# Optimization experiments

Hardware: AMD Instinct MI355X
Metric: run time of the kernel (lower is better)

## Reference

```python
import jax, jax.numpy as jnp
from jax import lax
import numpy as np

B, K_UP, K_DOWN = 32, 64, 192
D, S_UP, S_DOWN, C = 768, 24576, 24576, 256
CHUNK = 64  # connection chunk size (source uses 256; C=256 here, 4 chunks of 64)


def setup_inputs() -> dict:
    key = jax.random.key(0)
    k1, k2, k3, k4, k5, k6, k7 = jax.random.split(key, 7)
    up_decoder = jax.random.normal(k1, (D, S_UP), dtype=jnp.float32) * 0.02
    down_encoder = jax.random.normal(k2, (S_DOWN, D), dtype=jnp.float32) * 0.02
    up_b_dec = jax.random.normal(k3, (D,), dtype=jnp.float32) * 0.02
    up_vals = jax.random.normal(k4, (B, K_UP), dtype=jnp.float32)
    # connection table: indices of connected upstream features, -1 padded.
    conn = jax.random.randint(k5, (S_DOWN, C), 0, S_UP, dtype=jnp.int64)
    pad = jax.random.uniform(jax.random.fold_in(k5, 1), (S_DOWN, C)) < 0.25
    connections = jnp.where(pad, jnp.int64(-1), conn)
    up_indices = jax.random.randint(k6, (B, K_UP), 0, S_UP, dtype=jnp.int64)
    down_indices = jax.random.randint(k7, (B, K_DOWN), 0, S_DOWN, dtype=jnp.int64)
    return {"up_decoder": up_decoder, "down_encoder": down_encoder,
            "up_b_dec": up_b_dec, "up_vals": up_vals,
            "connections": connections, "up_indices": up_indices,
            "down_indices": down_indices}


def reference(up_decoder, down_encoder, up_b_dec, up_vals,
              connections, up_indices, down_indices):
    """JAX port of SCAESuite.get_pruned_contributions."""
    Bb, ku = up_indices.shape
    kd = down_indices.shape[1]
    Cc = connections.shape[1]
    # gather active upstream decoder columns -> [B, k_up, D]
    up_vecs = up_decoder.T[up_indices]
    # gather active downstream encoder rows -> [B, k_down, D]
    down_vecs = down_encoder[down_indices]
    # virtual weights [B, k_down, k_up]
    vw = jnp.einsum('bkd,bud->bku', down_vecs, up_vecs)
    # gather connection rows for each active downstream feature [B, k_down, C]
    conn_down = connections[down_indices]
    # scan over connection chunks, scatter-accumulating masked contributions
    chunks = conn_down.reshape(Bb, kd, Cc // CHUNK, CHUNK).transpose(2, 0, 1, 3)

    def body(acc, conn_chunk):  # conn_chunk [B, k_down, CHUNK]
        valid = conn_chunk != -1
        # match[b, kd, c, ku] = connection c of down feature equals active up feature
        match = (conn_chunk[..., None] == up_indices[:, None, None, :]) & valid[..., None]
        contrib = jnp.sum(
            jnp.where(match, vw[:, :, None, :] * up_vals[:, None, None, :], 0.0),
            axis=(2, 3))
        return acc + contrib, None

    contributions, _ = lax.scan(body, jnp.zeros((Bb, kd), up_vals.dtype), chunks)
    # upstream decoder bias contribution through downstream encoder
    b_dec_contrib = down_encoder @ up_b_dec  # [S_down]
    return contributions + b_dec_contrib[down_indices]
```

## Files before the change

### kernel.cpp

```cpp
#include <hip/hip_runtime.h>
#include <hip/hip_bf16.h>

#define B_SZ     32
#define K_UP     64
#define K_DOWN   192
#define D_DIM    768
#define S_UP     24576
#define C_CONN   256
#define NCOL     (B_SZ * K_UP)
#define MAXM     512
#define BM_WORDS (S_UP / 32)

#define CCH      512
#define RCH      16
#define NCH_C    (S_UP / CCH)
#define NCH_R    (D_DIM / RCH)
#define SLOTS    192

__global__ __launch_bounds__(256) void gather_up_cols_scan(
    const float* __restrict__ up_decoder,
    const int*   __restrict__ up_idx_flat,
    float*       __restrict__ ws_up)
{
    const int tid = threadIdx.x;
    const int c0  = blockIdx.x * CCH;
    const int d0  = blockIdx.y * RCH;

    __shared__ float tile[RCH][CCH + 4];
    __shared__ int   s_j[SLOTS];
    __shared__ int   s_cc[SLOTS];
    __shared__ int   s_cnt;

    if (tid == 0) s_cnt = 0;
    __syncthreads();

    for (int i = tid; i < NCOL; i += 256) {
        const int cc = up_idx_flat[i] - c0;
        if (cc >= 0 && cc < CCH) {
            int slot = atomicAdd(&s_cnt, 1);
            if (slot < SLOTS) { s_j[slot] = i; s_cc[slot] = cc; }
        }
    }

    #pragma unroll
    for (int k = 0; k < 8; ++k) {
        const int lin = k * 256 + tid;
        const int r   = lin >> 7;
        const int c4  = lin & 127;
        float4 v = *(const float4*)&up_decoder[(size_t)(d0 + r) * S_UP + c0 + c4 * 4];
        *(float4*)&tile[r][c4 * 4] = v;
    }
    __syncthreads();

    int cnt = s_cnt; if (cnt > SLOTS) cnt = SLOTS;

    const int q = tid & 3;
    for (int s = tid >> 2; s < cnt; s += 64) {
        const int j  = s_j[s];
        const int cc = s_cc[s];
        float4 v = make_float4(tile[4 * q + 0][cc], tile[4 * q + 1][cc],
                               tile[4 * q + 2][cc], tile[4 * q + 3][cc]);
        *(float4*)&ws_up[(size_t)j * D_DIM + d0 + 4 * q] = v;
    }
}

__global__ __launch_bounds__(256) void scae_pruned_contrib(
    const float* __restrict__ up_decoder,
    const float* __restrict__ ws_up,
    const float* __restrict__ down_encoder,
    const float* __restrict__ up_b_dec,
    const float* __restrict__ up_vals,
    const int*   __restrict__ connections,
    const int*   __restrict__ up_indices,
    const int*   __restrict__ down_indices,
    float*       __restrict__ out,
    const int                 use_ws)
{
    const int tid = threadIdx.x;
    const int blk = blockIdx.x;
    const int b   = blk / K_DOWN;
    const int kd  = blk - b * K_DOWN;

    __shared__ int      s_upidx[K_UP];
    __shared__ float    s_upvals[K_UP];
    __shared__ unsigned s_bm[BM_WORDS];
    __shared__ int      s_ku[MAXM];
    __shared__ float    s_coef[MAXM];
    __shared__ int      s_nm;
    __shared__ float    s_red[4];

    const int dj = down_indices[b * K_DOWN + kd];
    const int v  = connections[(size_t)dj * C_CONN + tid];

    const float* drow = down_encoder + (size_t)dj * D_DIM;
    const float dr0 = drow[tid];
    const float dr1 = drow[tid + 256];
    const float dr2 = drow[tid + 512];

    float c0 = up_b_dec[tid];
    float c1 = up_b_dec[tid + 256];
    float c2 = up_b_dec[tid + 512];

    int   ui = 0;
    float uv = 0.f;
    if (tid < K_UP) {
        ui = up_indices[b * K_UP + tid];
        uv = up_vals[b * K_UP + tid];
    }

    #pragma unroll
    for (int w = 0; w < BM_WORDS / 256; ++w) s_bm[tid + 256 * w] = 0u;
    if (tid == 0) s_nm = 0;
    if (tid < K_UP) { s_upidx[tid] = ui; s_upvals[tid] = uv; }
    __syncthreads();

    if (tid < K_UP) atomicOr(&s_bm[ui >> 5], 1u << (ui & 31));
    __syncthreads();

    if (v >= 0 && ((s_bm[v >> 5] >> (v & 31)) & 1u)) {
        for (int ku = 0; ku < K_UP; ++ku) {
            if (s_upidx[ku] == v) {
                int slot = atomicAdd(&s_nm, 1);
                if (slot < MAXM) {
                    s_ku[slot]   = ku;
                    s_coef[slot] = s_upvals[ku];
                }
            }
        }
    }
    __syncthreads();
    int nm = s_nm;
    if (nm > MAXM) nm = MAXM;

    for (int m = 0; m < nm; ++m) {
        const float coef = s_coef[m];
        const int   ku   = s_ku[m];
        if (use_ws) {
            const float* colp = ws_up + (size_t)(b * K_UP + ku) * D_DIM;
            c0 += coef * colp[tid];
            c1 += coef * colp[tid + 256];
            c2 += coef * colp[tid + 512];
        } else {
            const int col = s_upidx[ku];
            c0 += coef * up_decoder[(size_t)(tid      ) * S_UP + col];
            c1 += coef * up_decoder[(size_t)(tid + 256) * S_UP + col];
            c2 += coef * up_decoder[(size_t)(tid + 512) * S_UP + col];
        }
    }

    float partial = c0 * dr0 + c1 * dr1 + c2 * dr2;

    for (int off = 32; off > 0; off >>= 1)
        partial += __shfl_down(partial, off, 64);
    const int wave = tid >> 6;
    const int lane = tid & 63;
    if (lane == 0) s_red[wave] = partial;
    __syncthreads();
    if (tid == 0) {
        out[blk] = s_red[0] + s_red[1] + s_red[2] + s_red[3];
    }
}

extern "C" void kernel_launch(void* const* d_in, const int* in_sizes, int n_in,
                              void* d_out, int out_size, void* d_ws, size_t ws_size,
                              hipStream_t stream) {
    const float* up_decoder   = (const float*)d_in[0];
    const float* down_encoder = (const float*)d_in[1];
    const float* up_b_dec     = (const float*)d_in[2];
    const float* up_vals      = (const float*)d_in[3];
    const int*   connections  = (const int*)d_in[4];
    const int*   up_indices   = (const int*)d_in[5];
    const int*   down_indices = (const int*)d_in[6];
    float*       out          = (float*)d_out;
    float*       ws_up        = (float*)d_ws;

    const size_t ws_needed = (size_t)NCOL * D_DIM * sizeof(float);
    const int    use_ws    = (d_ws != nullptr && ws_size >= ws_needed) ? 1 : 0;

    if (use_ws) {
        gather_up_cols_scan<<<dim3(NCH_C, NCH_R), dim3(256), 0, stream>>>(
            up_decoder, up_indices, ws_up);
    }

    scae_pruned_contrib<<<dim3(B_SZ * K_DOWN), dim3(256), 0, stream>>>(
        up_decoder, ws_up, down_encoder, up_b_dec, up_vals,
        connections, up_indices, down_indices, out, use_ws);
}
```

Before: 187.9 us.

## Process eight downstream features per block and prefetch decoder tile before index scan

The main kernel now handles 8 downstream features per block instead of one. The per-batch setup work is shared across those features: clearing the 24K-bit bitmap, loading the upstream indices and values, and loading the bias. This cuts redundant shared-memory initialisation and gives each thread more independent loads. The gather kernel now issues its global float4 loads into registers before the index-scan loop, so load latency overlaps the scan. In exchange there are 8x fewer blocks (768), higher register pressure, and the match capacity per feature drops to 64.

```diff
diff --git a/kernel.cpp b/kernel.cpp
--- a/kernel.cpp
+++ b/kernel.cpp
@@ -8,8 +8,11 @@
 #define S_UP     24576
 #define C_CONN   256
 #define NCOL     (B_SZ * K_UP)
-#define MAXM     512
 #define BM_WORDS (S_UP / 32)
+
+#define KDB      8
+#define NGRP     (K_DOWN / KDB)
+#define MK       64
 
 #define CCH      512
 #define RCH      16
@@ -34,6 +37,15 @@
     if (tid == 0) s_cnt = 0;
     __syncthreads();
 
+    float4 v[8];
+    #pragma unroll
+    for (int k = 0; k < 8; ++k) {
+        const int lin = k * 256 + tid;
+        const int r   = lin >> 7;
+        const int c4  = lin & 127;
+        v[k] = *(const float4*)&up_decoder[(size_t)(d0 + r) * S_UP + c0 + c4 * 4];
+    }
+
     for (int i = tid; i < NCOL; i += 256) {
         const int cc = up_idx_flat[i] - c0;
         if (cc >= 0 && cc < CCH) {
@@ -47,8 +59,7 @@
         const int lin = k * 256 + tid;
         const int r   = lin >> 7;
         const int c4  = lin & 127;
-        float4 v = *(const float4*)&up_decoder[(size_t)(d0 + r) * S_UP + c0 + c4 * 4];
-        *(float4*)&tile[r][c4 * 4] = v;
+        *(float4*)&tile[r][c4 * 4] = v[k];
     }
     __syncthreads();
 
@@ -58,9 +69,9 @@
     for (int s = tid >> 2; s < cnt; s += 64) {
         const int j  = s_j[s];
         const int cc = s_cc[s];
-        float4 v = make_float4(tile[4 * q + 0][cc], tile[4 * q + 1][cc],
+        float4 w = make_float4(tile[4 * q + 0][cc], tile[4 * q + 1][cc],
                                tile[4 * q + 2][cc], tile[4 * q + 3][cc]);
-        *(float4*)&ws_up[(size_t)j * D_DIM + d0 + 4 * q] = v;
+        *(float4*)&ws_up[(size_t)j * D_DIM + d0 + 4 * q] = w;
     }
 }
 
@@ -78,28 +89,37 @@
 {
     const int tid = threadIdx.x;
     const int blk = blockIdx.x;
-    const int b   = blk / K_DOWN;
-    const int kd  = blk - b * K_DOWN;
+    const int b   = blk / NGRP;
+    const int g   = blk - b * NGRP;
+    const int kd0 = g * KDB;
 
     __shared__ int      s_upidx[K_UP];
     __shared__ float    s_upvals[K_UP];
     __shared__ unsigned s_bm[BM_WORDS];
-    __shared__ int      s_ku[MAXM];
-    __shared__ float    s_coef[MAXM];
-    __shared__ int      s_nm;
-    __shared__ float    s_red[4];
-
-    const int dj = down_indices[b * K_DOWN + kd];
-    const int v  = connections[(size_t)dj * C_CONN + tid];
-
-    const float* drow = down_encoder + (size_t)dj * D_DIM;
-    const float dr0 = drow[tid];
-    const float dr1 = drow[tid + 256];
-    const float dr2 = drow[tid + 512];
-
-    float c0 = up_b_dec[tid];
-    float c1 = up_b_dec[tid + 256];
-    float c2 = up_b_dec[tid + 512];
+    __shared__ int      s_ku[KDB][MK];
+    __shared__ float    s_coef[KDB][MK];
+    __shared__ int      s_nm[KDB];
+    __shared__ float    s_red[KDB][4];
+
+    int dj[KDB];
+    #pragma unroll
+    for (int k = 0; k < KDB; ++k)
+        dj[k] = down_indices[b * K_DOWN + kd0 + k];
+
+    int vv[KDB];
+    float dr0[KDB], dr1[KDB], dr2[KDB];
+    #pragma unroll
+    for (int k = 0; k < KDB; ++k) {
+        vv[k] = connections[(size_t)dj[k] * C_CONN + tid];
+        const float* drow = down_encoder + (size_t)dj[k] * D_DIM;
+        dr0[k] = drow[tid];
+        dr1[k] = drow[tid + 256];
+        dr2[k] = drow[tid + 512];
+    }
+
+    const float bd0 = up_b_dec[tid];
+    const float bd1 = up_b_dec[tid + 256];
+    const float bd2 = up_b_dec[tid + 512];
 
     int   ui = 0;
     float uv = 0.f;
@@ -110,54 +130,69 @@
 
     #pragma unroll
     for (int w = 0; w < BM_WORDS / 256; ++w) s_bm[tid + 256 * w] = 0u;
-    if (tid == 0) s_nm = 0;
+    if (tid < KDB) s_nm[tid] = 0;
     if (tid < K_UP) { s_upidx[tid] = ui; s_upvals[tid] = uv; }
     __syncthreads();
 
     if (tid < K_UP) atomicOr(&s_bm[ui >> 5], 1u << (ui & 31));
     __syncthreads();
 
-    if (v >= 0 && ((s_bm[v >> 5] >> (v & 31)) & 1u)) {
-        for (int ku = 0; ku < K_UP; ++ku) {
-            if (s_upidx[ku] == v) {
-                int slot = atomicAdd(&s_nm, 1);
-                if (slot < MAXM) {
-                    s_ku[slot]   = ku;
-                    s_coef[slot] = s_upvals[ku];
+    #pragma unroll
+    for (int k = 0; k < KDB; ++k) {
+        const int v = vv[k];
+        if (v >= 0 && ((s_bm[v >> 5] >> (v & 31)) & 1u)) {
+            for (int ku = 0; ku < K_UP; ++ku) {
+                if (s_upidx[ku] == v) {
+                    int slot = atomicAdd(&s_nm[k], 1);
+                    if (slot < MK) {
+                        s_ku[k][slot]   = ku;
+                        s_coef[k][slot] = s_upvals[ku];
+                    }
                 }
             }
         }
     }
     __syncthreads();
-    int nm = s_nm;
-    if (nm > MAXM) nm = MAXM;
-
-    for (int m = 0; m < nm; ++m) {
-        const float coef = s_coef[m];
-        const int   ku   = s_ku[m];
-        if (use_ws) {
-            const float* colp = ws_up + (size_t)(b * K_UP + ku) * D_DIM;
-            c0 += coef * colp[tid];
-            c1 += coef * colp[tid + 256];
-            c2 += coef * colp[tid + 512];
-        } else {
-            const int col = s_upidx[ku];
-            c0 += coef * up_decoder[(size_t)(tid      ) * S_UP + col];
-            c1 += coef * up_decoder[(size_t)(tid + 256) * S_UP + col];
-            c2 += coef * up_decoder[(size_t)(tid + 512) * S_UP + col];
+
+    float p[KDB];
+    #pragma unroll
+    for (int k = 0; k < KDB; ++k) {
+        int nm = s_nm[k];
+        if (nm > MK) nm = MK;
+
+        float c0 = bd0, c1 = bd1, c2 = bd2;
+        for (int m = 0; m < nm; ++m) {
+            const float coef = s_coef[k][m];
+            const int   ku   = s_ku[k][m];
+            if (use_ws) {
+                const float* colp = ws_up + (size_t)(b * K_UP + ku) * D_DIM;
+                c0 += coef * colp[tid];
+                c1 += coef * colp[tid + 256];
+                c2 += coef * colp[tid + 512];
+            } else {
+                const int col = s_upidx[ku];
+                c0 += coef * up_decoder[(size_t)(tid      ) * S_UP + col];
+                c1 += coef * up_decoder[(size_t)(tid + 256) * S_UP + col];
+                c2 += coef * up_decoder[(size_t)(tid + 512) * S_UP + col];
+            }
         }
-    }
-
-    float partial = c0 * dr0 + c1 * dr1 + c2 * dr2;
-
-    for (int off = 32; off > 0; off >>= 1)
-        partial += __shfl_down(partial, off, 64);
+        p[k] = c0 * dr0[k] + c1 * dr1[k] + c2 * dr2[k];
+    }
+
     const int wave = tid >> 6;
     const int lane = tid & 63;
-    if (lane == 0) s_red[wave] = partial;
-    __syncthreads();
-    if (tid == 0) {
-        out[blk] = s_red[0] + s_red[1] + s_red[2] + s_red[3];
+    #pragma unroll
+    for (int k = 0; k < KDB; ++k) {
+        float r = p[k];
+        for (int off = 32; off > 0; off >>= 1)
+            r += __shfl_down(r, off, 64);
+        if (lane == 0) s_red[k][wave] = r;
+    }
+    __syncthreads();
+
+    if (tid < KDB) {
+        out[b * K_DOWN + kd0 + tid] =
+            s_red[tid][0] + s_red[tid][1] + s_red[tid][2] + s_red[tid][3];
     }
 }
 
@@ -182,7 +217,7 @@
             up_decoder, up_indices, ws_up);
     }
 
-    scae_pruned_contrib<<<dim3(B_SZ * K_DOWN), dim3(256), 0, stream>>>(
+    scae_pruned_contrib<<<dim3(B_SZ * (K_DOWN / KDB)), dim3(256), 0, stream>>>(
         up_decoder, ws_up, down_encoder, up_b_dec, up_vals,
         connections, up_indices, down_indices, out, use_ws);
 }
```

Result: slower. 200.8 us (+6.9%).
